# Performance work log

Hardware: AMD Instinct MI355X
Metric: run time of the kernel (lower is better)

The kernel has to match this reference:

```python
import jax, jax.numpy as jnp
import numpy as np

D_MODEL = 1024
NUM_HEADS = 16
HEAD_DIM = D_MODEL // NUM_HEADS
SCALE = 1.0 / np.sqrt(HEAD_DIM).astype(np.float32)


def setup_inputs() -> dict:
    key = jax.random.key(0)
    k1, k2, k3, k4 = jax.random.split(key, 4)
    B, L = 1, 4096
    s = 0.02
    x = jax.random.normal(k1, (B, L, D_MODEL), dtype=jnp.float32)
    W_qkv = jax.random.normal(k2, (D_MODEL, 3 * D_MODEL), dtype=jnp.float32) * s
    W_o = jax.random.normal(k3, (D_MODEL, D_MODEL), dtype=jnp.float32) * s
    b_o = jax.random.normal(k4, (D_MODEL,), dtype=jnp.float32) * s
    return {"x": x, "W_qkv": W_qkv, "W_o": W_o, "b_o": b_o}


def reference(x, W_qkv, W_o, b_o):
    B, L, D = x.shape
    H, Hd = NUM_HEADS, HEAD_DIM
    qkv = x @ W_qkv                          # [B, L, 3D]
    qkv = qkv.reshape(B, L, 3, H, Hd)
    q = jnp.transpose(qkv[:, :, 0], (0, 2, 1, 3))  # [B, H, L, Hd]
    k = jnp.transpose(qkv[:, :, 1], (0, 2, 1, 3))
    v = jnp.transpose(qkv[:, :, 2], (0, 2, 1, 3))
    scores = jnp.einsum("bhqd,bhkd->bhqk", q, k) * SCALE  # [B, H, L, L]
    attn = jax.nn.softmax(scores, axis=-1)
    out = jnp.einsum("bhqk,bhkd->bhqd", attn, v)          # [B, H, L, Hd]
    out = jnp.transpose(out, (0, 2, 1, 3)).reshape(B, L, D)
    return out @ W_o + b_o
```

## Files before the change

kernel.cpp:

```cpp
#include <hip/hip_runtime.h>
#include <stdint.h>


#define L_SEQ 4096
#define DM 1024
#define NHEAD 16
#define HDIM 64
#define ATT_SCALE 0.125f
#define LOG2E 1.4426950408889634f
#define CSC (ATT_SCALE * LOG2E)

typedef __attribute__((ext_vector_type(8))) __bf16 bf16x8;
typedef __attribute__((ext_vector_type(4))) __bf16 bf16x4;
typedef __attribute__((ext_vector_type(4))) float f32x4;
typedef __attribute__((ext_vector_type(8))) float f32x8;
typedef __attribute__((ext_vector_type(4))) short short4v;
typedef __attribute__((ext_vector_type(8))) short short8v;

#define GLL16(g, l) __builtin_amdgcn_global_load_lds( \
    (__attribute__((address_space(1))) void*)(g),     \
    (__attribute__((address_space(3))) void*)(l), 16, 0, 0)

#define MFMA32(a, b, c) __builtin_amdgcn_mfma_f32_16x16x32_bf16((a), (b), (c), 0, 0, 0)

__device__ __forceinline__ short f2bf(float f) {
  uint32_t u = __builtin_bit_cast(uint32_t, f);
  u += 0x7fffu + ((u >> 16) & 1u);
  return (short)(u >> 16);
}

__global__ __launch_bounds__(256)
void prep_kernel(const float* __restrict__ x, short* __restrict__ xb,
                 const float* __restrict__ Wq, short* __restrict__ wqt,
                 const float* __restrict__ Wo, short* __restrict__ wot) {
  __shared__ __align__(16) short tbuf[64 * 66];
  const int tid = threadIdx.x;
  const int blk = blockIdx.x;
  if (blk < 4096) {
    int i = blk * 256 + tid;
    float4 v = ((const float4*)x)[i];
    short4 o;
    o.x = f2bf(v.x); o.y = f2bf(v.y); o.z = f2bf(v.z); o.w = f2bf(v.w);
    ((short4*)xb)[i] = o;
    return;
  }
  const float* W; short* Wt; int N, nb, kb;
  const int K = 1024;
  if (blk < 4096 + 768) {
    int b = blk - 4096;
    W = Wq; Wt = wqt; N = 3072; nb = (b % 48) * 64; kb = (b / 48) * 64;
  } else {
    int b = blk - (4096 + 768);
    W = Wo; Wt = wot; N = 1024; nb = (b % 16) * 64; kb = (b / 16) * 64;
  }
#pragma unroll
  for (int i = 0; i < 16; i++) {
    int idx = tid + i * 256;
    int r = idx >> 6, c = idx & 63;
    tbuf[r * 66 + c] = f2bf(W[(size_t)(kb + r) * N + nb + c]);
  }
  __syncthreads();
#pragma unroll
  for (int i = 0; i < 16; i++) {
    int idx = tid + i * 256;
    int r = idx >> 6, c = idx & 63;
    Wt[(size_t)(nb + r) * K + kb + c] = tbuf[c * 66 + r];
  }
}

__global__ __launch_bounds__(256, 2)
void gemm_qkv(const short* __restrict__ A, const short* __restrict__ Bt,
              short* __restrict__ qkv, short* __restrict__ vtout, int K) {
  __shared__ __align__(16) short smem[16384];
  short* As = smem;
  short* Bs = smem + 8192;
  const int tid = threadIdx.x;
  const int lane = tid & 63;
  const int wave = tid >> 6;
  const int quad = lane >> 4;
  const int cl = lane & 15;
  const int m0 = blockIdx.x * 128;
  const int n0 = blockIdx.y * 128;
  const int wm = (wave >> 1) * 64;
  const int wn = (wave & 1) * 64;

  f32x4 acc[4][4] = {};

  for (int kb = 0; kb < K; kb += 64) {
    __syncthreads();
#pragma unroll
    for (int i = 0; i < 4; i++) {
      int ci = i * 256 + tid;
      int row = ci & 127, c = ci >> 7;
      GLL16(A + (size_t)(m0 + row) * K + kb + c * 8, As + ci * 8);
      GLL16(Bt + (size_t)(n0 + row) * K + kb + c * 8, Bs + ci * 8);
    }
    __syncthreads();
#pragma unroll
    for (int ks = 0; ks < 2; ks++) {
      bf16x8 af[4], bfr[4];
#pragma unroll
      for (int t = 0; t < 4; t++) {
        af[t]  = *(const bf16x8*)(As + ((ks * 4 + quad) * 128 + wm + t * 16 + cl) * 8);
        bfr[t] = *(const bf16x8*)(Bs + ((ks * 4 + quad) * 128 + wn + t * 16 + cl) * 8);
      }
#pragma unroll
      for (int mt = 0; mt < 4; mt++)
#pragma unroll
        for (int nt = 0; nt < 4; nt++)
          acc[mt][nt] = MFMA32(af[mt], bfr[nt], acc[mt][nt]);
    }
  }

  const int which = n0 >> 10;
  if (which == 2) {
#pragma unroll
    for (int mt = 0; mt < 4; mt++)
#pragma unroll
      for (int nt = 0; nt < 4; nt++) {
        int col = n0 + wn + nt * 16 + cl;
        int hd = col & 63;
        int hidx = (col >> 6) & 15;
        int row0 = m0 + wm + mt * 16 + quad * 4;
        short4v pk;
#pragma unroll
        for (int r = 0; r < 4; r++) pk[r] = f2bf(acc[mt][nt][r]);
        *(short4v*)(vtout + ((size_t)hidx * HDIM + hd) * L_SEQ + row0) = pk;
      }
  } else {
    const float sc = (which == 0) ? CSC : 1.0f;
    short* Ct = smem;
#pragma unroll
    for (int p = 0; p < 2; p++) {
      __syncthreads();
      if ((wave & 1) == p) {
#pragma unroll
        for (int mt = 0; mt < 4; mt++)
#pragma unroll
          for (int nt = 0; nt < 4; nt++) {
            int m = wm + mt * 16 + quad * 4;
            int c = nt * 16 + cl;
#pragma unroll
            for (int r = 0; r < 4; r++)
              Ct[(m + r) * 72 + c] = f2bf(acc[mt][nt][r] * sc);
          }
      }
      __syncthreads();
      int hidx = ((n0 + p * 64) >> 6) & 15;
      size_t base = ((size_t)which * NHEAD + hidx) * L_SEQ * HDIM;
      int m = tid >> 1;
      int j0 = (tid & 1) * 4;
#pragma unroll
      for (int i = 0; i < 4; i++) {
        short8v v = *(const short8v*)(Ct + m * 72 + (j0 + i) * 8);
        *(short8v*)(qkv + base + (size_t)(m0 + m) * HDIM + (j0 + i) * 8) = v;
      }
    }
  }
}

__global__ __launch_bounds__(256, 2)
void gemm_out(const short* __restrict__ A, const short* __restrict__ Bt,
              float* __restrict__ C, const float* __restrict__ bias, int K) {
  __shared__ __align__(16) short As[4096];
  __shared__ __align__(16) short Bs[2048];
  const int tid = threadIdx.x;
  const int lane = tid & 63;
  const int wave = tid >> 6;
  const int quad = lane >> 4;
  const int cl = lane & 15;
  const int m0 = blockIdx.x * 128;
  const int n0 = blockIdx.y * 64;
  const int wm = (wave >> 1) * 64;
  const int wn = (wave & 1) * 32;
  const int N = 1024;

  f32x4 acc[4][2] = {};

  for (int kb = 0; kb < K; kb += 32) {
    __syncthreads();
#pragma unroll
    for (int i = 0; i < 2; i++) {
      int ci = i * 256 + tid;
      GLL16(A + (size_t)(m0 + (ci & 127)) * K + kb + (ci >> 7) * 8, As + ci * 8);
    }
    GLL16(Bt + (size_t)(n0 + (tid & 63)) * K + kb + (tid >> 6) * 8, Bs + tid * 8);
    __syncthreads();
    bf16x8 af[4], bfr[2];
#pragma unroll
    for (int t = 0; t < 4; t++)
      af[t] = *(const bf16x8*)(As + (quad * 128 + wm + t * 16 + cl) * 8);
#pragma unroll
    for (int t = 0; t < 2; t++)
      bfr[t] = *(const bf16x8*)(Bs + (quad * 64 + wn + t * 16 + cl) * 8);
#pragma unroll
    for (int mt = 0; mt < 4; mt++)
#pragma unroll
      for (int nt = 0; nt < 2; nt++)
        acc[mt][nt] = MFMA32(af[mt], bfr[nt], acc[mt][nt]);
  }

#pragma unroll
  for (int mt = 0; mt < 4; mt++)
#pragma unroll
    for (int nt = 0; nt < 2; nt++) {
      int col = n0 + wn + nt * 16 + cl;
      float b = bias[col];
#pragma unroll
      for (int r = 0; r < 4; r++) {
        int row = m0 + wm + mt * 16 + quad * 4 + r;
        C[(size_t)row * N + col] = acc[mt][nt][r] + b;
      }
    }
}

#define KVB 128
__global__ __launch_bounds__(512, 4)
void attn_kernel(const short* __restrict__ qkv, const short* __restrict__ vt,
                 short* __restrict__ aout) {
  __shared__ __align__(16) short Ks[2][KVB * HDIM];
  __shared__ __align__(16) short Vs[2][HDIM * KVB];
  __shared__ float lbuf[512];
  const int tid = threadIdx.x, lane = tid & 63, wave = tid >> 6;
  const int quad = lane >> 4, cl = lane & 15;
  const int kg = wave & 1;
  const int qg = wave >> 1;
  const int bid = blockIdx.x;
  const int h  = ((bid & 7) << 1) | ((bid >> 3) & 1);
  const int qb = bid >> 4;
  const short* Qg = qkv + (size_t)h * L_SEQ * HDIM;
  const short* Kg = qkv + ((size_t)NHEAD + h) * L_SEQ * HDIM;
  const short* Vg = vt + (size_t)h * HDIM * L_SEQ;
  const int keyoff = ((cl >> 2) << 3) | (cl & 3);

  bf16x8 qf[2][2];
#pragma unroll
  for (int qs = 0; qs < 2; qs++) {
    int qrow = qb * 128 + qg * 32 + qs * 16 + cl;
    qf[qs][0] = *(const bf16x8*)(Qg + (size_t)qrow * HDIM + quad * 8);
    qf[qs][1] = *(const bf16x8*)(Qg + (size_t)qrow * HDIM + 32 + quad * 8);
  }
  const short8v ov = {0x3F80, 0x3F80, 0x3F80, 0x3F80, 0x3F80, 0x3F80, 0x3F80, 0x3F80};
  const bf16x8 ones = __builtin_bit_cast(bf16x8, ov);
  f32x4 o_l[2] = {};
  f32x4 o_acc[4][2] = {};

  int koff[2][2][2];
  int voff[2][4];
#pragma unroll
  for (int kslab = 0; kslab < 2; kslab++) {
#pragma unroll
    for (int b = 0; b < 2; b++) {
      int krow = kg * 64 + kslab * 32 + keyoff + b * 4;
      int sw = (krow & 3) | (((krow >> 3) & 1) << 2);
#pragma unroll
      for (int ks = 0; ks < 2; ks++)
        koff[kslab][b][ks] = (krow * 8 + ((ks * 4 + quad) ^ sw)) * 8;
    }
#pragma unroll
    for (int G = 0; G < 4; G++) {
      int vrow = G * 16 + cl;
      int sw = (vrow & 3) | (((vrow >> 3) & 1) << 2);
      voff[kslab][G] = ((kg * 64 + vrow) * 8 + ((kslab * 4 + quad) ^ sw)) * 8;
    }
  }

  const short* kp[2]; const short* vp[2]; int ldsoK[2], ldsoV[2];
#pragma unroll
  for (int i = 0; i < 2; i++) {
    int ciK = i * 512 + tid;
    int rowK = ciK >> 3;
    int swK = (rowK & 3) | (((rowK >> 3) & 1) << 2);
    int cK = (ciK & 7) ^ swK;
    kp[i] = Kg + (size_t)rowK * HDIM + cK * 8;
    ldsoK[i] = ciK * 8;
    int ciV = i * 512 + tid;
    int half = ciV >> 9;
    int hd = (ciV >> 3) & 63;
    int cp = ciV & 7;
    int swV = (hd & 3) | (((hd >> 3) & 1) << 2);
    vp[i] = Vg + (size_t)hd * L_SEQ + (half * 8 + (cp ^ swV)) * 8;
    ldsoV[i] = ciV * 8;
  }
#define STAGE(t, buf)                                        \
  {                                                          \
    _Pragma("unroll")                                        \
    for (int i = 0; i < 2; i++) {                            \
      GLL16(kp[i] + (t) * KVB * HDIM, &Ks[buf][ldsoK[i]]);   \
      GLL16(vp[i] + (t) * KVB, &Vs[buf][ldsoV[i]]);          \
    }                                                        \
  }

  STAGE(0, 0);
#pragma unroll 2
  for (int t = 0; t < L_SEQ / KVB; t++) {
    const int cur = t & 1;
    __syncthreads();
    if (t + 1 < L_SEQ / KVB) STAGE(t + 1, cur ^ 1);
    const short* Kb = Ks[cur];
    const short* Vb = Vs[cur];

#pragma unroll
    for (int kslab = 0; kslab < 2; kslab++) {
      f32x4 s[2][2] = {};
      __builtin_amdgcn_s_setprio(1);
#pragma unroll
      for (int b = 0; b < 2; b++)
#pragma unroll
        for (int ks = 0; ks < 2; ks++) {
          bf16x8 kf = *(const bf16x8*)(Kb + koff[kslab][b][ks]);
#pragma unroll
          for (int qs = 0; qs < 2; qs++)
            s[qs][b] = MFMA32(kf, qf[qs][ks], s[qs][b]);
        }
      __builtin_amdgcn_s_setprio(0);

      bf16x8 vfr[4];
#pragma unroll
      for (int G = 0; G < 4; G++)
        vfr[G] = *(const bf16x8*)(Vb + voff[kslab][G]);

      bf16x8 pb0;
      {
        f32x8 pv8;
#pragma unroll
        for (int b = 0; b < 2; b++)
#pragma unroll
          for (int r = 0; r < 4; r++)
            pv8[b * 4 + r] = __builtin_amdgcn_exp2f(s[0][b][r]);
        pb0 = __builtin_convertvector(pv8, bf16x8);
      }

      __builtin_amdgcn_s_setprio(1);
      o_l[0] = MFMA32(ones, pb0, o_l[0]);
#pragma unroll
      for (int G = 0; G < 4; G++)
        o_acc[G][0] = MFMA32(vfr[G], pb0, o_acc[G][0]);
      __builtin_amdgcn_s_setprio(0);

      bf16x8 pb1;
      {
        f32x8 pv8;
#pragma unroll
        for (int b = 0; b < 2; b++)
#pragma unroll
          for (int r = 0; r < 4; r++)
            pv8[b * 4 + r] = __builtin_amdgcn_exp2f(s[1][b][r]);
        pb1 = __builtin_convertvector(pv8, bf16x8);
      }

      __builtin_amdgcn_s_setprio(1);
      o_l[1] = MFMA32(ones, pb1, o_l[1]);
#pragma unroll
      for (int G = 0; G < 4; G++)
        o_acc[G][1] = MFMA32(vfr[G], pb1, o_acc[G][1]);
      __builtin_amdgcn_s_setprio(0);
    }
  }
#undef STAGE

  __syncthreads();
  float* ored = (float*)&Ks[0][0];
  if (kg == 1) {
#pragma unroll
    for (int G = 0; G < 4; G++)
#pragma unroll
      for (int qs = 0; qs < 2; qs++)
        *(f32x4*)&ored[(((qg * 4 + G) * 2 + qs) * 64 + lane) * 4] = o_acc[G][qs];
#pragma unroll
    for (int qs = 0; qs < 2; qs++)
      lbuf[(qg * 2 + qs) * 64 + lane] = o_l[qs][0];
  }
  __syncthreads();
  if (kg == 0) {
#pragma unroll
    for (int qs = 0; qs < 2; qs++) {
      float l = o_l[qs][0] + lbuf[(qg * 2 + qs) * 64 + lane];
      float inv = 1.f / l;
      int token = qb * 128 + qg * 32 + qs * 16 + cl;
#pragma unroll
      for (int G = 0; G < 4; G++) {
        f32x4 part = *(const f32x4*)&ored[(((qg * 4 + G) * 2 + qs) * 64 + lane) * 4];
        f32x4 sc = (o_acc[G][qs] + part) * inv;
        bf16x4 pk = __builtin_convertvector(sc, bf16x4);
        *(short4v*)(aout + (size_t)token * DM + h * HDIM + G * 16 + quad * 4) =
            __builtin_bit_cast(short4v, pk);
      }
    }
  }
}

extern "C" void kernel_launch(void* const* d_in, const int* in_sizes, int n_in,
                              void* d_out, int out_size, void* d_ws, size_t ws_size,
                              hipStream_t stream) {
  const float* x    = (const float*)d_in[0];
  const float* Wqkv = (const float*)d_in[1];
  const float* Wo   = (const float*)d_in[2];
  const float* bo   = (const float*)d_in[3];
  char* ws = (char*)d_ws;
  short* xb    = (short*)(ws);
  short* wqkvt = (short*)(ws + (size_t)8 * 1024 * 1024);
  short* wot   = (short*)(ws + (size_t)14 * 1024 * 1024);
  short* qkv   = (short*)(ws + (size_t)16 * 1024 * 1024);
  short* vt    = (short*)(ws + (size_t)40 * 1024 * 1024);
  short* aout  = xb;
  float* out = (float*)d_out;

  prep_kernel<<<4096 + 768 + 256, 256, 0, stream>>>(x, xb, Wqkv, wqkvt, Wo, wot);
  gemm_qkv<<<dim3(32, 24), 256, 0, stream>>>(xb, wqkvt, qkv, vt, DM);
  attn_kernel<<<dim3(512), 512, 0, stream>>>(qkv, vt, aout);
  gemm_out<<<dim3(32, 16), 256, 0, stream>>>(aout, wot, out, bo, DM);
}
```

Baseline: 236.7 us.

## Double K-step in output GEMM and reschedule attention inner loop for overlap

The output-projection GEMM now loads 64-wide K slabs per iteration instead of 32, which halves the number of barrier pairs. Its LDS footprint grows accordingly. The attention inner loop is restructured so both kslab score computations are issued back to back with K fragments preloaded. The exp/convert of one slab is interleaved with the V loads and PV MFMAs of the other, aiming to overlap VALU exp work with matrix ops. This raises register pressure, which may affect occupancy under the 512-thread, 4-block bound.

```diff
diff --git a/kernel.cpp b/kernel.cpp
--- a/kernel.cpp
+++ b/kernel.cpp
@@ -162,8 +162,8 @@
 __global__ __launch_bounds__(256, 2)
 void gemm_out(const short* __restrict__ A, const short* __restrict__ Bt,
               float* __restrict__ C, const float* __restrict__ bias, int K) {
-  __shared__ __align__(16) short As[4096];
-  __shared__ __align__(16) short Bs[2048];
+  __shared__ __align__(16) short As[8192];
+  __shared__ __align__(16) short Bs[4096];
   const int tid = threadIdx.x;
   const int lane = tid & 63;
   const int wave = tid >> 6;
@@ -177,27 +177,34 @@
 
   f32x4 acc[4][2] = {};
 
-  for (int kb = 0; kb < K; kb += 32) {
+  for (int kb = 0; kb < K; kb += 64) {
     __syncthreads();
+#pragma unroll
+    for (int i = 0; i < 4; i++) {
+      int ci = i * 256 + tid;
+      GLL16(A + (size_t)(m0 + (ci & 127)) * K + kb + (ci >> 7) * 8, As + ci * 8);
+    }
 #pragma unroll
     for (int i = 0; i < 2; i++) {
       int ci = i * 256 + tid;
-      GLL16(A + (size_t)(m0 + (ci & 127)) * K + kb + (ci >> 7) * 8, As + ci * 8);
-    }
-    GLL16(Bt + (size_t)(n0 + (tid & 63)) * K + kb + (tid >> 6) * 8, Bs + tid * 8);
+      GLL16(Bt + (size_t)(n0 + (ci & 63)) * K + kb + (ci >> 6) * 8, Bs + ci * 8);
+    }
     __syncthreads();
-    bf16x8 af[4], bfr[2];
-#pragma unroll
-    for (int t = 0; t < 4; t++)
-      af[t] = *(const bf16x8*)(As + (quad * 128 + wm + t * 16 + cl) * 8);
-#pragma unroll
-    for (int t = 0; t < 2; t++)
-      bfr[t] = *(const bf16x8*)(Bs + (quad * 64 + wn + t * 16 + cl) * 8);
-#pragma unroll
-    for (int mt = 0; mt < 4; mt++)
-#pragma unroll
-      for (int nt = 0; nt < 2; nt++)
-        acc[mt][nt] = MFMA32(af[mt], bfr[nt], acc[mt][nt]);
+#pragma unroll
+    for (int ks = 0; ks < 2; ks++) {
+      bf16x8 af[4], bfr[2];
+#pragma unroll
+      for (int t = 0; t < 4; t++)
+        af[t] = *(const bf16x8*)(As + ((ks * 4 + quad) * 128 + wm + t * 16 + cl) * 8);
+#pragma unroll
+      for (int t = 0; t < 2; t++)
+        bfr[t] = *(const bf16x8*)(Bs + ((ks * 4 + quad) * 64 + wn + t * 16 + cl) * 8);
+#pragma unroll
+      for (int mt = 0; mt < 4; mt++)
+#pragma unroll
+        for (int nt = 0; nt < 2; nt++)
+          acc[mt][nt] = MFMA32(af[mt], bfr[nt], acc[mt][nt]);
+    }
   }
 
 #pragma unroll
@@ -300,62 +307,92 @@
     const short* Kb = Ks[cur];
     const short* Vb = Vs[cur];
 
-#pragma unroll
-    for (int kslab = 0; kslab < 2; kslab++) {
-      f32x4 s[2][2] = {};
-      __builtin_amdgcn_s_setprio(1);
+    f32x4 s[2][2][2];
+    bf16x8 kf0[2][2];
+#pragma unroll
+    for (int b = 0; b < 2; b++)
+#pragma unroll
+      for (int ks = 0; ks < 2; ks++)
+        kf0[b][ks] = *(const bf16x8*)(Kb + koff[0][b][ks]);
+    __builtin_amdgcn_s_setprio(1);
+#pragma unroll
+    for (int b = 0; b < 2; b++)
+#pragma unroll
+      for (int ks = 0; ks < 2; ks++)
+#pragma unroll
+        for (int qs = 0; qs < 2; qs++)
+          s[0][qs][b] = MFMA32(kf0[b][ks], qf[qs][ks],
+                               (ks == 0) ? (f32x4){} : s[0][qs][b]);
+    __builtin_amdgcn_s_setprio(0);
+    bf16x8 kf1[2][2];
+#pragma unroll
+    for (int b = 0; b < 2; b++)
+#pragma unroll
+      for (int ks = 0; ks < 2; ks++)
+        kf1[b][ks] = *(const bf16x8*)(Kb + koff[1][b][ks]);
+    __builtin_amdgcn_s_setprio(1);
+#pragma unroll
+    for (int b = 0; b < 2; b++)
+#pragma unroll
+      for (int ks = 0; ks < 2; ks++)
+#pragma unroll
+        for (int qs = 0; qs < 2; qs++)
+          s[1][qs][b] = MFMA32(kf1[b][ks], qf[qs][ks],
+                               (ks == 0) ? (f32x4){} : s[1][qs][b]);
+    __builtin_amdgcn_s_setprio(0);
+
+    bf16x8 vfr[4];
+#pragma unroll
+    for (int G = 0; G < 4; G++)
+      vfr[G] = *(const bf16x8*)(Vb + voff[0][G]);
+
+    bf16x8 p0[2];
+#pragma unroll
+    for (int qs = 0; qs < 2; qs++) {
+      f32x8 pv8;
 #pragma unroll
       for (int b = 0; b < 2; b++)
 #pragma unroll
-        for (int ks = 0; ks < 2; ks++) {
-          bf16x8 kf = *(const bf16x8*)(Kb + koff[kslab][b][ks]);
-#pragma unroll
-          for (int qs = 0; qs < 2; qs++)
-            s[qs][b] = MFMA32(kf, qf[qs][ks], s[qs][b]);
-        }
-      __builtin_amdgcn_s_setprio(0);
-
-      bf16x8 vfr[4];
+        for (int r = 0; r < 4; r++)
+          pv8[b * 4 + r] = __builtin_amdgcn_exp2f(s[0][qs][b][r]);
+      p0[qs] = __builtin_convertvector(pv8, bf16x8);
+    }
+
+    __builtin_amdgcn_s_setprio(1);
+#pragma unroll
+    for (int qs = 0; qs < 2; qs++) {
+      o_l[qs] = MFMA32(ones, p0[qs], o_l[qs]);
 #pragma unroll
       for (int G = 0; G < 4; G++)
-        vfr[G] = *(const bf16x8*)(Vb + voff[kslab][G]);
-
-      bf16x8 pb0;
-      {
-        f32x8 pv8;
-#pragma unroll
-        for (int b = 0; b < 2; b++)
-#pragma unroll
-          for (int r = 0; r < 4; r++)
-            pv8[b * 4 + r] = __builtin_amdgcn_exp2f(s[0][b][r]);
-        pb0 = __builtin_convertvector(pv8, bf16x8);
-      }
-
-      __builtin_amdgcn_s_setprio(1);
-      o_l[0] = MFMA32(ones, pb0, o_l[0]);
+        o_acc[G][qs] = MFMA32(vfr[G], p0[qs], o_acc[G][qs]);
+    }
+    __builtin_amdgcn_s_setprio(0);
+
+    bf16x8 p1[2];
+#pragma unroll
+    for (int qs = 0; qs < 2; qs++) {
+      f32x8 pv8;
+#pragma unroll
+      for (int b = 0; b < 2; b++)
+#pragma unroll
+        for (int r = 0; r < 4; r++)
+          pv8[b * 4 + r] = __builtin_amdgcn_exp2f(s[1][qs][b][r]);
+      p1[qs] = __builtin_convertvector(pv8, bf16x8);
+    }
+
+#pragma unroll
+    for (int G = 0; G < 4; G++)
+      vfr[G] = *(const bf16x8*)(Vb + voff[1][G]);
+
+    __builtin_amdgcn_s_setprio(1);
+#pragma unroll
+    for (int qs = 0; qs < 2; qs++) {
+      o_l[qs] = MFMA32(ones, p1[qs], o_l[qs]);
 #pragma unroll
       for (int G = 0; G < 4; G++)
-        o_acc[G][0] = MFMA32(vfr[G], pb0, o_acc[G][0]);
-      __builtin_amdgcn_s_setprio(0);
-
-      bf16x8 pb1;
-      {
-        f32x8 pv8;
-#pragma unroll
-        for (int b = 0; b < 2; b++)
-#pragma unroll
-          for (int r = 0; r < 4; r++)
-            pv8[b * 4 + r] = __builtin_amdgcn_exp2f(s[1][b][r]);
-        pb1 = __builtin_convertvector(pv8, bf16x8);
-      }
-
-      __builtin_amdgcn_s_setprio(1);
-      o_l[1] = MFMA32(ones, pb1, o_l[1]);
-#pragma unroll
-      for (int G = 0; G < 4; G++)
-        o_acc[G][1] = MFMA32(vfr[G], pb1, o_acc[G][1]);
-      __builtin_amdgcn_s_setprio(0);
-    }
+        o_acc[G][qs] = MFMA32(vfr[G], p1[qs], o_acc[G][qs]);
+    }
+    __builtin_amdgcn_s_setprio(0);
   }
 #undef STAGE
 
```

Result: slower. 245.1 us (+3.5%).

## Double-buffer LDS in QKV and output GEMMs and relayout V tile in attention

Applied to the files above, without the earlier changes.

Both GEMM kernels switch from single-buffered LDS with two barriers per step to double-buffered LDS, prefetching the next K tile while computing the current one with one barrier per iteration. The output GEMM also grows its K step from 32 to 64. The attention kernel changes how the V^T tile is laid out in LDS: each head-dim row now holds 16 key chunks contiguously, which makes global reads longer and changes the swizzle. In exchange, LDS use doubles, which may limit occupancy, and the GEMM loops are unrolled further.

```diff
diff --git a/kernel.cpp b/kernel.cpp
--- a/kernel.cpp
+++ b/kernel.cpp
@@ -71,9 +71,11 @@
 __global__ __launch_bounds__(256, 2)
 void gemm_qkv(const short* __restrict__ A, const short* __restrict__ Bt,
               short* __restrict__ qkv, short* __restrict__ vtout, int K) {
-  __shared__ __align__(16) short smem[16384];
-  short* As = smem;
-  short* Bs = smem + 8192;
+  __shared__ __align__(16) short smem[32768];
+  short* const As0 = smem;
+  short* const As1 = smem + 8192;
+  short* const Bs0 = smem + 16384;
+  short* const Bs1 = smem + 24576;
   const int tid = threadIdx.x;
   const int lane = tid & 63;
   const int wave = tid >> 6;
@@ -86,23 +88,41 @@
 
   f32x4 acc[4][4] = {};
 
-  for (int kb = 0; kb < K; kb += 64) {
+  const short* ap[4]; const short* bp[4]; int lo[4];
+#pragma unroll
+  for (int i = 0; i < 4; i++) {
+    int ci = i * 256 + tid;
+    int row = ci & 127, c = ci >> 7;
+    ap[i] = A + (size_t)(m0 + row) * K + c * 8;
+    bp[i] = Bt + (size_t)(n0 + row) * K + c * 8;
+    lo[i] = ci * 8;
+  }
+#define QSTAGE(kt, As_, Bs_)                         \
+  {                                                  \
+    _Pragma("unroll")                                \
+    for (int i = 0; i < 4; i++) {                    \
+      GLL16(ap[i] + (kt) * 64, (As_) + lo[i]);       \
+      GLL16(bp[i] + (kt) * 64, (Bs_) + lo[i]);       \
+    }                                                \
+  }
+
+  const int NT = K >> 6;
+  QSTAGE(0, As0, Bs0);
+#pragma unroll 2
+  for (int kt = 0; kt < NT; kt++) {
+    short* Ac = (kt & 1) ? As1 : As0;
+    short* Bc = (kt & 1) ? Bs1 : Bs0;
+    short* An = (kt & 1) ? As0 : As1;
+    short* Bn = (kt & 1) ? Bs0 : Bs1;
     __syncthreads();
-#pragma unroll
-    for (int i = 0; i < 4; i++) {
-      int ci = i * 256 + tid;
-      int row = ci & 127, c = ci >> 7;
-      GLL16(A + (size_t)(m0 + row) * K + kb + c * 8, As + ci * 8);
-      GLL16(Bt + (size_t)(n0 + row) * K + kb + c * 8, Bs + ci * 8);
-    }
-    __syncthreads();
+    if (kt + 1 < NT) QSTAGE(kt + 1, An, Bn);
 #pragma unroll
     for (int ks = 0; ks < 2; ks++) {
       bf16x8 af[4], bfr[4];
 #pragma unroll
       for (int t = 0; t < 4; t++) {
-        af[t]  = *(const bf16x8*)(As + ((ks * 4 + quad) * 128 + wm + t * 16 + cl) * 8);
-        bfr[t] = *(const bf16x8*)(Bs + ((ks * 4 + quad) * 128 + wn + t * 16 + cl) * 8);
+        af[t]  = *(const bf16x8*)(Ac + ((ks * 4 + quad) * 128 + wm + t * 16 + cl) * 8);
+        bfr[t] = *(const bf16x8*)(Bc + ((ks * 4 + quad) * 128 + wn + t * 16 + cl) * 8);
       }
 #pragma unroll
       for (int mt = 0; mt < 4; mt++)
@@ -111,6 +131,7 @@
           acc[mt][nt] = MFMA32(af[mt], bfr[nt], acc[mt][nt]);
     }
   }
+#undef QSTAGE
 
   const int which = n0 >> 10;
   if (which == 2) {
@@ -162,8 +183,11 @@
 __global__ __launch_bounds__(256, 2)
 void gemm_out(const short* __restrict__ A, const short* __restrict__ Bt,
               float* __restrict__ C, const float* __restrict__ bias, int K) {
-  __shared__ __align__(16) short As[4096];
-  __shared__ __align__(16) short Bs[2048];
+  __shared__ __align__(16) short smem[24576];
+  short* const As0 = smem;
+  short* const As1 = smem + 8192;
+  short* const Bs0 = smem + 16384;
+  short* const Bs1 = smem + 20480;
   const int tid = threadIdx.x;
   const int lane = tid & 63;
   const int wave = tid >> 6;
@@ -177,28 +201,56 @@
 
   f32x4 acc[4][2] = {};
 
-  for (int kb = 0; kb < K; kb += 32) {
+  const short* ap[4]; const short* bp[2]; int loA[4], loB[2];
+#pragma unroll
+  for (int i = 0; i < 4; i++) {
+    int ci = i * 256 + tid;
+    ap[i] = A + (size_t)(m0 + (ci & 127)) * K + (ci >> 7) * 8;
+    loA[i] = ci * 8;
+  }
+#pragma unroll
+  for (int i = 0; i < 2; i++) {
+    int ci = i * 256 + tid;
+    bp[i] = Bt + (size_t)(n0 + (ci & 63)) * K + (ci >> 6) * 8;
+    loB[i] = ci * 8;
+  }
+#define OSTAGE(kt, As_, Bs_)                          \
+  {                                                   \
+    _Pragma("unroll")                                 \
+    for (int i = 0; i < 4; i++)                       \
+      GLL16(ap[i] + (kt) * 64, (As_) + loA[i]);       \
+    _Pragma("unroll")                                 \
+    for (int i = 0; i < 2; i++)                       \
+      GLL16(bp[i] + (kt) * 64, (Bs_) + loB[i]);       \
+  }
+
+  const int NT = K >> 6;
+  OSTAGE(0, As0, Bs0);
+#pragma unroll 2
+  for (int kt = 0; kt < NT; kt++) {
+    short* Ac = (kt & 1) ? As1 : As0;
+    short* Bc = (kt & 1) ? Bs1 : Bs0;
+    short* An = (kt & 1) ? As0 : As1;
+    short* Bn = (kt & 1) ? Bs0 : Bs1;
     __syncthreads();
-#pragma unroll
-    for (int i = 0; i < 2; i++) {
-      int ci = i * 256 + tid;
-      GLL16(A + (size_t)(m0 + (ci & 127)) * K + kb + (ci >> 7) * 8, As + ci * 8);
-    }
-    GLL16(Bt + (size_t)(n0 + (tid & 63)) * K + kb + (tid >> 6) * 8, Bs + tid * 8);
-    __syncthreads();
-    bf16x8 af[4], bfr[2];
-#pragma unroll
-    for (int t = 0; t < 4; t++)
-      af[t] = *(const bf16x8*)(As + (quad * 128 + wm + t * 16 + cl) * 8);
-#pragma unroll
-    for (int t = 0; t < 2; t++)
-      bfr[t] = *(const bf16x8*)(Bs + (quad * 64 + wn + t * 16 + cl) * 8);
-#pragma unroll
-    for (int mt = 0; mt < 4; mt++)
-#pragma unroll
-      for (int nt = 0; nt < 2; nt++)
-        acc[mt][nt] = MFMA32(af[mt], bfr[nt], acc[mt][nt]);
-  }
+    if (kt + 1 < NT) OSTAGE(kt + 1, An, Bn);
+#pragma unroll
+    for (int ks = 0; ks < 2; ks++) {
+      bf16x8 af[4], bfr[2];
+#pragma unroll
+      for (int t = 0; t < 4; t++)
+        af[t] = *(const bf16x8*)(Ac + ((ks * 4 + quad) * 128 + wm + t * 16 + cl) * 8);
+#pragma unroll
+      for (int t = 0; t < 2; t++)
+        bfr[t] = *(const bf16x8*)(Bc + ((ks * 4 + quad) * 64 + wn + t * 16 + cl) * 8);
+#pragma unroll
+      for (int mt = 0; mt < 4; mt++)
+#pragma unroll
+        for (int nt = 0; nt < 2; nt++)
+          acc[mt][nt] = MFMA32(af[mt], bfr[nt], acc[mt][nt]);
+    }
+  }
+#undef OSTAGE
 
 #pragma unroll
   for (int mt = 0; mt < 4; mt++)
@@ -261,7 +313,7 @@
     for (int G = 0; G < 4; G++) {
       int vrow = G * 16 + cl;
       int sw = (vrow & 3) | (((vrow >> 3) & 1) << 2);
-      voff[kslab][G] = ((kg * 64 + vrow) * 8 + ((kslab * 4 + quad) ^ sw)) * 8;
+      voff[kslab][G] = (vrow * 16 + ((kg * 8 + kslab * 4 + quad) ^ sw)) * 8;
     }
   }
 
@@ -275,11 +327,10 @@
     kp[i] = Kg + (size_t)rowK * HDIM + cK * 8;
     ldsoK[i] = ciK * 8;
     int ciV = i * 512 + tid;
-    int half = ciV >> 9;
-    int hd = (ciV >> 3) & 63;
-    int cp = ciV & 7;
-    int swV = (hd & 3) | (((hd >> 3) & 1) << 2);
-    vp[i] = Vg + (size_t)hd * L_SEQ + (half * 8 + (cp ^ swV)) * 8;
+    int rowV = ciV >> 4;
+    int swV = (rowV & 3) | (((rowV >> 3) & 1) << 2);
+    int cV = (ciV & 15) ^ swV;
+    vp[i] = Vg + (size_t)rowV * L_SEQ + cV * 8;
     ldsoV[i] = ciV * 8;
   }
 #define STAGE(t, buf)                                        \
```

After: 236.8 us. About the same (+0.0%).

## Triple-buffer GEMM LDS loads with async waitcnt pipelining and relayout V tile

Applied to the files above, without the earlier changes.

Both projection GEMMs now keep a three-stage LDS ring with a K-step of 32. Loads for tile t+2 are issued before computing tile t, and the old double __syncthreads is replaced by a single s_waitcnt vmcnt plus s_barrier per iteration, so global latency overlaps MFMA work. The QKV GEMM occupancy hint rises to 3 blocks per CU. Separately, the attention kernel's V^T tile now uses a row-of-16-chunks layout with a matching swizzle, which changes the LDS read and write offsets. The main risks are correctness of the vmcnt counts and the new swizzle, plus extra LDS use.

```diff
diff --git a/kernel.cpp b/kernel.cpp
--- a/kernel.cpp
+++ b/kernel.cpp
@@ -68,12 +68,10 @@
   }
 }
 
-__global__ __launch_bounds__(256, 2)
+__global__ __launch_bounds__(256, 3)
 void gemm_qkv(const short* __restrict__ A, const short* __restrict__ Bt,
               short* __restrict__ qkv, short* __restrict__ vtout, int K) {
-  __shared__ __align__(16) short smem[16384];
-  short* As = smem;
-  short* Bs = smem + 8192;
+  __shared__ __align__(16) short smem[24576];
   const int tid = threadIdx.x;
   const int lane = tid & 63;
   const int wave = tid >> 6;
@@ -86,31 +84,58 @@
 
   f32x4 acc[4][4] = {};
 
-  for (int kb = 0; kb < K; kb += 64) {
-    __syncthreads();
-#pragma unroll
-    for (int i = 0; i < 4; i++) {
-      int ci = i * 256 + tid;
-      int row = ci & 127, c = ci >> 7;
-      GLL16(A + (size_t)(m0 + row) * K + kb + c * 8, As + ci * 8);
-      GLL16(Bt + (size_t)(n0 + row) * K + kb + c * 8, Bs + ci * 8);
-    }
-    __syncthreads();
-#pragma unroll
-    for (int ks = 0; ks < 2; ks++) {
-      bf16x8 af[4], bfr[4];
-#pragma unroll
-      for (int t = 0; t < 4; t++) {
-        af[t]  = *(const bf16x8*)(As + ((ks * 4 + quad) * 128 + wm + t * 16 + cl) * 8);
-        bfr[t] = *(const bf16x8*)(Bs + ((ks * 4 + quad) * 128 + wn + t * 16 + cl) * 8);
-      }
-#pragma unroll
-      for (int mt = 0; mt < 4; mt++)
-#pragma unroll
-        for (int nt = 0; nt < 4; nt++)
-          acc[mt][nt] = MFMA32(af[mt], bfr[nt], acc[mt][nt]);
-    }
-  }
+  const short* ap[2]; const short* bp[2]; int lo[2];
+#pragma unroll
+  for (int i = 0; i < 2; i++) {
+    int ci = i * 256 + tid;
+    int row = ci & 127, c = ci >> 7;
+    ap[i] = A + (size_t)(m0 + row) * K + c * 8;
+    bp[i] = Bt + (size_t)(n0 + row) * K + c * 8;
+    lo[i] = ci * 8;
+  }
+  short* pA0 = smem;          short* pA1 = smem + 4096;   short* pA2 = smem + 8192;
+  short* pB0 = smem + 12288;  short* pB1 = smem + 16384;  short* pB2 = smem + 20480;
+#define QST(kt, Ab, Bb)                              \
+  {                                                  \
+    _Pragma("unroll")                                \
+    for (int i = 0; i < 2; i++) {                    \
+      GLL16(ap[i] + (kt) * 32, (Ab) + lo[i]);        \
+      GLL16(bp[i] + (kt) * 32, (Bb) + lo[i]);        \
+    }                                                \
+  }
+#define QCOMP(Ab, Bb)                                                          \
+  {                                                                            \
+    bf16x8 af[4], bfr[4];                                                      \
+    _Pragma("unroll")                                                          \
+    for (int t4 = 0; t4 < 4; t4++) {                                           \
+      af[t4]  = *(const bf16x8*)((Ab) + (quad * 128 + wm + t4 * 16 + cl) * 8); \
+      bfr[t4] = *(const bf16x8*)((Bb) + (quad * 128 + wn + t4 * 16 + cl) * 8); \
+    }                                                                          \
+    _Pragma("unroll")                                                          \
+    for (int mt = 0; mt < 4; mt++)                                             \
+      _Pragma("unroll")                                                        \
+      for (int nt = 0; nt < 4; nt++)                                           \
+        acc[mt][nt] = MFMA32(af[mt], bfr[nt], acc[mt][nt]);                    \
+  }
+
+  const int NT = K >> 5;
+  QST(0, pA0, pB0);
+  QST(1, pA1, pB1);
+  for (int t = 0; t < NT - 1; t++) {
+    asm volatile("s_waitcnt vmcnt(4)" ::: "memory");
+    __builtin_amdgcn_s_barrier();
+    __builtin_amdgcn_sched_barrier(0);
+    if (t + 2 < NT) QST(t + 2, pA2, pB2);
+    QCOMP(pA0, pB0);
+    short* tA = pA0; pA0 = pA1; pA1 = pA2; pA2 = tA;
+    short* tB = pB0; pB0 = pB1; pB1 = pB2; pB2 = tB;
+  }
+  asm volatile("s_waitcnt vmcnt(0)" ::: "memory");
+  __builtin_amdgcn_s_barrier();
+  __builtin_amdgcn_sched_barrier(0);
+  QCOMP(pA0, pB0);
+#undef QST
+#undef QCOMP
 
   const int which = n0 >> 10;
   if (which == 2) {
@@ -162,8 +187,7 @@
 __global__ __launch_bounds__(256, 2)
 void gemm_out(const short* __restrict__ A, const short* __restrict__ Bt,
               float* __restrict__ C, const float* __restrict__ bias, int K) {
-  __shared__ __align__(16) short As[4096];
-  __shared__ __align__(16) short Bs[2048];
+  __shared__ __align__(16) short smem[18432];
   const int tid = threadIdx.x;
   const int lane = tid & 63;
   const int wave = tid >> 6;
@@ -177,28 +201,58 @@
 
   f32x4 acc[4][2] = {};
 
-  for (int kb = 0; kb < K; kb += 32) {
-    __syncthreads();
-#pragma unroll
-    for (int i = 0; i < 2; i++) {
-      int ci = i * 256 + tid;
-      GLL16(A + (size_t)(m0 + (ci & 127)) * K + kb + (ci >> 7) * 8, As + ci * 8);
-    }
-    GLL16(Bt + (size_t)(n0 + (tid & 63)) * K + kb + (tid >> 6) * 8, Bs + tid * 8);
-    __syncthreads();
-    bf16x8 af[4], bfr[2];
-#pragma unroll
-    for (int t = 0; t < 4; t++)
-      af[t] = *(const bf16x8*)(As + (quad * 128 + wm + t * 16 + cl) * 8);
-#pragma unroll
-    for (int t = 0; t < 2; t++)
-      bfr[t] = *(const bf16x8*)(Bs + (quad * 64 + wn + t * 16 + cl) * 8);
-#pragma unroll
-    for (int mt = 0; mt < 4; mt++)
-#pragma unroll
-      for (int nt = 0; nt < 2; nt++)
-        acc[mt][nt] = MFMA32(af[mt], bfr[nt], acc[mt][nt]);
-  }
+  const short* ap[2]; const short* bp1; int loA[2], loB;
+#pragma unroll
+  for (int i = 0; i < 2; i++) {
+    int ci = i * 256 + tid;
+    ap[i] = A + (size_t)(m0 + (ci & 127)) * K + (ci >> 7) * 8;
+    loA[i] = ci * 8;
+  }
+  bp1 = Bt + (size_t)(n0 + (tid & 63)) * K + (tid >> 6) * 8;
+  loB = tid * 8;
+  short* pA0 = smem;          short* pA1 = smem + 4096;   short* pA2 = smem + 8192;
+  short* pB0 = smem + 12288;  short* pB1 = smem + 14336;  short* pB2 = smem + 16384;
+#define OST(kt, Ab, Bb)                              \
+  {                                                  \
+    _Pragma("unroll")                                \
+    for (int i = 0; i < 2; i++)                      \
+      GLL16(ap[i] + (kt) * 32, (Ab) + loA[i]);       \
+    GLL16(bp1 + (kt) * 32, (Bb) + loB);              \
+  }
+#define OCOMP(Ab, Bb)                                                          \
+  {                                                                            \
+    bf16x8 af[4], bfr[2];                                                      \
+    _Pragma("unroll")                                                          \
+    for (int t4 = 0; t4 < 4; t4++)                                             \
+      af[t4] = *(const bf16x8*)((Ab) + (quad * 128 + wm + t4 * 16 + cl) * 8);  \
+    _Pragma("unroll")                                                          \
+    for (int t4 = 0; t4 < 2; t4++)                                             \
+      bfr[t4] = *(const bf16x8*)((Bb) + (quad * 64 + wn + t4 * 16 + cl) * 8);  \
+    _Pragma("unroll")                                                          \
+    for (int mt = 0; mt < 4; mt++)                                             \
+      _Pragma("unroll")                                                        \
+      for (int nt = 0; nt < 2; nt++)                                           \
+        acc[mt][nt] = MFMA32(af[mt], bfr[nt], acc[mt][nt]);                    \
+  }
+
+  const int NT = K >> 5;
+  OST(0, pA0, pB0);
+  OST(1, pA1, pB1);
+  for (int t = 0; t < NT - 1; t++) {
+    asm volatile("s_waitcnt vmcnt(3)" ::: "memory");
+    __builtin_amdgcn_s_barrier();
+    __builtin_amdgcn_sched_barrier(0);
+    if (t + 2 < NT) OST(t + 2, pA2, pB2);
+    OCOMP(pA0, pB0);
+    short* tA = pA0; pA0 = pA1; pA1 = pA2; pA2 = tA;
+    short* tB = pB0; pB0 = pB1; pB1 = pB2; pB2 = tB;
+  }
+  asm volatile("s_waitcnt vmcnt(0)" ::: "memory");
+  __builtin_amdgcn_s_barrier();
+  __builtin_amdgcn_sched_barrier(0);
+  OCOMP(pA0, pB0);
+#undef OST
+#undef OCOMP
 
 #pragma unroll
   for (int mt = 0; mt < 4; mt++)
@@ -261,7 +315,7 @@
     for (int G = 0; G < 4; G++) {
       int vrow = G * 16 + cl;
       int sw = (vrow & 3) | (((vrow >> 3) & 1) << 2);
-      voff[kslab][G] = ((kg * 64 + vrow) * 8 + ((kslab * 4 + quad) ^ sw)) * 8;
+      voff[kslab][G] = (vrow * 16 + ((kg * 8 + kslab * 4 + quad) ^ sw)) * 8;
     }
   }
 
@@ -275,11 +329,10 @@
     kp[i] = Kg + (size_t)rowK * HDIM + cK * 8;
     ldsoK[i] = ciK * 8;
     int ciV = i * 512 + tid;
-    int half = ciV >> 9;
-    int hd = (ciV >> 3) & 63;
-    int cp = ciV & 7;
-    int swV = (hd & 3) | (((hd >> 3) & 1) << 2);
-    vp[i] = Vg + (size_t)hd * L_SEQ + (half * 8 + (cp ^ swV)) * 8;
+    int rowV = ciV >> 4;
+    int swV = (rowV & 3) | (((rowV >> 3) & 1) << 2);
+    int cV = (ciV & 15) ^ swV;
+    vp[i] = Vg + (size_t)rowV * L_SEQ + cV * 8;
     ldsoV[i] = ciV * 8;
   }
 #define STAGE(t, buf)                                        \
```

After: 231.8 us, median of 3. -2.1%, faster.
